# Performance work log

Measured on AMD Instinct MI355X. Metric: run time of the kernel, lower is better.

Reference implementation:

```python
import jax, jax.numpy as jnp
import numpy as np

REF_MIC_IDX = 0
LOAD = 0.001 / np.sqrt(2.0)  # diagonal loading added to BOTH real and imag parts in the torch code


def setup_inputs() -> dict:
    key = jax.random.key(0)
    k1, k2, k3 = jax.random.split(key, 3)
    shape = (8, 2, 8, 600, 257)  # N, RI, C, T, F
    return {
        "mixture": jax.random.normal(k1, shape, dtype=jnp.float32),
        "target": jax.random.normal(k2, shape, dtype=jnp.float32),
        "noise": jax.random.normal(k3, shape, dtype=jnp.float32),
    }


def _to_complex(x):
    # (N, 2, C, T, F) RI-stacked -> (N, C, T, F) complex
    return jax.lax.complex(x[:, 0], x[:, 1])


def reference(mixture, target, noise):
    N, _, C, T, F = mixture.shape
    y = _to_complex(mixture)  # (N, C, T, F)
    v = _to_complex(noise)
    cdtype = y.dtype

    # Time-averaged spatial covariance: sum_t V V^H / T -> (N, F, C, C)
    # (fused; the original materializes per-frame C x C matrices then sums)
    phi_v = jnp.einsum("nctf,ndtf->nfcd", v, jnp.conj(v)) / T
    phi_y = jnp.einsum("nctf,ndtf->nfcd", y, jnp.conj(y)) / T

    eye = jnp.eye(C, dtype=cdtype)
    # torch adds LOAD*eye to both real and imag slices -> complex (1+1j)*LOAD*eye
    phi_v = phi_v + (LOAD * (1.0 + 1.0j)) * eye

    G = jnp.linalg.inv(phi_v) @ phi_y  # (N, F, C, C)

    # l = trace(G) - C, where torch subtracts scalar C from both RI parts
    l = jnp.trace(G, axis1=-2, axis2=-1) - (C * (1.0 + 1.0j))  # (N, F)

    # H = (1/l) * (G - I) e_ref  -> column ref_mic_idx of (G - I)
    Ge = (G - eye)[..., :, REF_MIC_IDX]  # (N, F, C)
    H = Ge / l[..., None]  # (N, F, C)

    # Beamform: X(n,t,f) = sum_c conj(H)_{n,f,c} * y_{n,c,t,f}
    X = jnp.einsum("nfc,nctf->ntf", jnp.conj(H), y)  # (N, T, F)

    # Output in RI-stacked form with singleton channel: (N, 2, 1, T, F)
    est = jnp.stack([jnp.real(X), jnp.imag(X)], axis=1)[:, :, None]
    return est
```

## Files before the change

### kernel.cpp

```cpp
#include <hip/hip_runtime.h>


constexpr int N_  = 8;
constexpr int C_  = 8;
constexpr int T_  = 600;
constexpr int F_  = 257;
constexpr int TF_  = T_ * F_;
constexpr int CTF_ = C_ * TF_;
constexpr int NSTR_ = 2 * CTF_;
constexpr int NF_  = N_ * F_;
constexpr int NPAIR_ = 36;
constexpr float LOADC_ = 7.0710678118654755e-4f;
constexpr float INV_T_ = 1.0f / 600.0f;

struct cx { float r, i; };
__device__ __forceinline__ cx cmul(cx a, cx b) { return {a.r*b.r - a.i*b.i, a.r*b.i + a.i*b.r}; }
__device__ __forceinline__ cx csub(cx a, cx b) { return {a.r - b.r, a.i - b.i}; }
__device__ __forceinline__ cx cconj(cx a) { return {a.r, -a.i}; }
__device__ __forceinline__ cx cinv(cx a) {
    float id = 1.0f / (a.r*a.r + a.i*a.i);
    return {a.r*id, -a.i*id};
}
__device__ __forceinline__ cx cmadd(cx acc, cx a, cx b) {
    acc.r += a.r*b.r - a.i*b.i;
    acc.i += a.r*b.i + a.i*b.r;
    return acc;
}

template<int TSPLIT>
__global__ __launch_bounds__(64, 1) void cov_partial(
        const float* __restrict__ mix, const float* __restrict__ noi,
        float* __restrict__ part) {
    constexpr int TCHUNK = T_ / TSPLIT;
    constexpr int PIPE = 4;
    static_assert(TCHUNK > PIPE, "pipeline deeper than chunk");

    int f = blockIdx.x * 64 + threadIdx.x;
    if (f >= F_) return;
    int n = blockIdx.y;
    int z = blockIdx.z;
    int m = z & 1;
    int chunk = z >> 1;
    const float* src = m ? mix : noi;
    const float* pt = src + (size_t)n * NSTR_ + f + (size_t)(chunk * TCHUNK) * F_;

    float reB[PIPE][C_], imB[PIPE][C_];
#pragma unroll
    for (int s = 0; s < PIPE; ++s) {
        const float* pn = pt + (size_t)s * F_;
#pragma unroll
        for (int c = 0; c < C_; ++c) {
            reB[s][c] = pn[(size_t)c * TF_];
            imB[s][c] = pn[(size_t)c * TF_ + CTF_];
        }
    }

    float accr[NPAIR_], acci[NPAIR_];
#pragma unroll
    for (int p = 0; p < NPAIR_; ++p) { accr[p] = 0.f; acci[p] = 0.f; }

#pragma unroll
    for (int tt = 0; tt < TCHUNK; ++tt) {
        const int s = tt % PIPE;
        float re[C_], im[C_];
#pragma unroll
        for (int c = 0; c < C_; ++c) { re[c] = reB[s][c]; im[c] = imB[s][c]; }

        if (tt + PIPE < TCHUNK) {
            const float* pn = pt + (size_t)(tt + PIPE) * F_;
#pragma unroll
            for (int c = 0; c < C_; ++c) {
                reB[s][c] = pn[(size_t)c * TF_];
                imB[s][c] = pn[(size_t)c * TF_ + CTF_];
            }
        }

        int p = 0;
#pragma unroll
        for (int c = 0; c < C_; ++c) {
#pragma unroll
            for (int d = 0; d <= c; ++d, ++p) {
                accr[p] += re[c]*re[d] + im[c]*im[d];
                acci[p] += im[c]*re[d] - re[c]*im[d];
            }
        }
    }

    float* out = part + (size_t)((m * TSPLIT + chunk) * 72) * NF_ + n * F_ + f;
#pragma unroll
    for (int p = 0; p < NPAIR_; ++p) {
        out[(size_t)(2*p)   * NF_] = accr[p];
        out[(size_t)(2*p+1) * NF_] = acci[p];
    }
}

__global__ __launch_bounds__(256) void reduce_cov(float* __restrict__ part, int tsplit) {
    int flat = blockIdx.x * 256 + threadIdx.x;
    constexpr int NQ4 = NF_ / 4;
    if (flat >= 2 * 72 * NQ4) return;
    int idx4 = flat % NQ4;
    int z = flat / NQ4;
    int m = z / 72;
    int q = z % 72;
    const float4* p4 = (const float4*)(part) + ((size_t)((m * tsplit) * 72 + q) * NF_) / 4 + idx4;
    float4 s = {0.f, 0.f, 0.f, 0.f};
    for (int ch = 0; ch < tsplit; ++ch) {
        float4 v = p4[(size_t)(ch * 72) * NF_ / 4];
        s.x += v.x; s.y += v.y; s.z += v.z; s.w += v.w;
    }
    *(float4*)((float*)part + (size_t)((m * tsplit) * 72 + q) * NF_ + idx4 * 4) = s;
}

__global__ __launch_bounds__(64, 1) void solve_w(
        const float* __restrict__ part, float* __restrict__ W, size_t yBase) {
    int idx = blockIdx.x * 64 + threadIdx.x;
    if (idx >= NF_) return;

    const float* pv = part + idx;
    const float* py = part + yBase + idx;

    cx M[64];
#pragma unroll
    for (int c = 0; c < 8; ++c) {
#pragma unroll
        for (int d = 0; d <= c; ++d) {
            int p = c*(c+1)/2 + d;
            cx val = { pv[(size_t)(2*p) * NF_] * INV_T_,
                       pv[(size_t)(2*p+1) * NF_] * INV_T_ };
            if (d == c) { val.r += LOADC_; val.i += LOADC_; }
            M[c*8 + d] = val;
            if (d < c) M[d*8 + c] = cconj(val);
        }
    }

#pragma unroll
    for (int k = 0; k < 8; ++k) {
        cx p = cinv(M[k*8 + k]);
        M[k*8 + k] = p;
#pragma unroll
        for (int j = 0; j < 8; ++j) {
            if (j != k) M[k*8 + j] = cmul(M[k*8 + j], p);
        }
#pragma unroll
        for (int i = 0; i < 8; ++i) {
            if (i == k) continue;
            cx fkt = M[i*8 + k];
#pragma unroll
            for (int j = 0; j < 8; ++j) {
                if (j != k) M[i*8 + j] = csub(M[i*8 + j], cmul(fkt, M[k*8 + j]));
            }
            cx t = cmul(fkt, p);
            M[i*8 + k] = { -t.r, -t.i };
        }
    }

    cx tr = {0.f, 0.f};
    cx g0[8];
#pragma unroll
    for (int c = 0; c < 8; ++c) g0[c] = (cx){0.f, 0.f};

#pragma unroll
    for (int a = 0; a < 8; ++a) {
#pragma unroll
        for (int b = 0; b <= a; ++b) {
            int p = a*(a+1)/2 + b;
            cx yv = { py[(size_t)(2*p) * NF_] * INV_T_,
                      py[(size_t)(2*p+1) * NF_] * INV_T_ };
            tr = cmadd(tr, M[b*8 + a], yv);
            if (a != b) tr = cmadd(tr, M[a*8 + b], cconj(yv));
            if (b == 0) {
#pragma unroll
                for (int i = 0; i < 8; ++i) g0[i] = cmadd(g0[i], M[i*8 + a], yv);
            }
        }
    }

    cx l = { tr.r - 8.0f, tr.i - 8.0f };
    float iden = 1.0f / (l.r*l.r + l.i*l.i);

    float* w = W + (size_t)idx * 16;
#pragma unroll
    for (int c = 0; c < 8; ++c) {
        cx ge = g0[c];
        if (c == 0) ge.r -= 1.0f;
        w[2*c]     = (ge.r*l.r + ge.i*l.i) * iden;
        w[2*c + 1] = (ge.r*l.i - ge.i*l.r) * iden;
    }
}

__global__ __launch_bounds__(256) void beamform(
        const float* __restrict__ mix, const float* __restrict__ W,
        float* __restrict__ out) {
    int n = blockIdx.y;
    int j = blockIdx.x * 256 + threadIdx.x;
    if (j >= TF_) return;
    int f = j % F_;

    const float4* w4 = (const float4*)(W + (size_t)(n * F_ + f) * 16);
    float4 q0 = w4[0], q1 = w4[1], q2 = w4[2], q3 = w4[3];
    float wv[16] = { q0.x, q0.y, q0.z, q0.w,
                     q1.x, q1.y, q1.z, q1.w,
                     q2.x, q2.y, q2.z, q2.w,
                     q3.x, q3.y, q3.z, q3.w };

    const float* base = mix + (size_t)n * NSTR_ + j;
    float xr = 0.f, xi = 0.f;
#pragma unroll
    for (int c = 0; c < C_; ++c) {
        float yr = base[(size_t)c * TF_];
        float yi = base[(size_t)c * TF_ + CTF_];
        float wr = wv[2*c], wi = wv[2*c + 1];
        xr += wr*yr - wi*yi;
        xi += wr*yi + wi*yr;
    }
    float* op = out + (size_t)n * (2 * TF_);
    op[j]       = xr;
    op[TF_ + j] = xi;
}

extern "C" void kernel_launch(void* const* d_in, const int* in_sizes, int n_in,
                              void* d_out, int out_size, void* d_ws, size_t ws_size,
                              hipStream_t stream) {
    const float* mix = (const float*)d_in[0];
    const float* noi = (const float*)d_in[2];

    const size_t need25 = ((size_t)2 * 25 * 72 * NF_ + (size_t)16 * NF_) * 4;
    float* part = (float*)d_ws;
    int tsplit;
    if (ws_size >= need25) {
        tsplit = 25;
        cov_partial<25><<<dim3(5, N_, 2 * 25), 64, 0, stream>>>(mix, noi, part);
    } else {
        tsplit = 15;
        cov_partial<15><<<dim3(5, N_, 2 * 15), 64, 0, stream>>>(mix, noi, part);
    }
    float* W = part + (size_t)2 * tsplit * 72 * NF_;

    reduce_cov<<<dim3((2 * 72 * (NF_ / 4) + 255) / 256), 256, 0, stream>>>(part, tsplit);
    solve_w<<<dim3((NF_ + 63) / 64), 64, 0, stream>>>(part, W, (size_t)tsplit * 72 * NF_);
    beamform<<<dim3((TF_ + 255) / 256, N_), 256, 0, stream>>>(mix, W, (float*)d_out);
}
```

Measured before the change: 281.6 us.

## Stream covariance inputs through an async global-to-LDS ring buffer

The covariance kernel used to prefetch four time frames into registers. It now issues direct global-to-LDS loads into a three-stage shared-memory ring, with manual vmcnt and lgkmcnt waits between stages. The intent is to keep more loads in flight per wave while freeing registers held by the prefetch buffers, since this one-wave-per-block kernel is bound by memory latency. The fallback time split changes from 15 to 20 so the chunk length divides evenly by the ring depth. The trade-off is hand-written wait counts that must match the number of loads each stage issues, which is fragile, plus extra LDS read traffic.

```diff
diff --git a/kernel.cpp b/kernel.cpp
--- a/kernel.cpp
+++ b/kernel.cpp
@@ -1,4 +1,5 @@
 #include <hip/hip_runtime.h>
+#include <stdint.h>
 
 
 constexpr int N_  = 8;
@@ -27,54 +28,57 @@
     return acc;
 }
 
+__device__ __forceinline__ void gload_lds4(const float* g, float* l) {
+    __builtin_amdgcn_global_load_lds(
+        (const __attribute__((address_space(1))) void*)g,
+        (__attribute__((address_space(3))) void*)l,
+        4, 0, 0);
+}
+
+#define VMWAIT(N) asm volatile("s_waitcnt vmcnt(" #N ")" ::: "memory")
+#define LGKM0()   asm volatile("s_waitcnt lgkmcnt(0)" ::: "memory")
+
 template<int TSPLIT>
 __global__ __launch_bounds__(64, 1) void cov_partial(
         const float* __restrict__ mix, const float* __restrict__ noi,
         float* __restrict__ part) {
     constexpr int TCHUNK = T_ / TSPLIT;
-    constexpr int PIPE = 4;
-    static_assert(TCHUNK > PIPE, "pipeline deeper than chunk");
-
-    int f = blockIdx.x * 64 + threadIdx.x;
+    constexpr int P = 3;
+    static_assert(TCHUNK % P == 0 && TCHUNK > P, "ring/chunk mismatch");
+
+    __shared__ float S[P][16][64];
+
+    const int lane = threadIdx.x;
+    const int f = blockIdx.x * 64 + lane;
     if (f >= F_) return;
-    int n = blockIdx.y;
-    int z = blockIdx.z;
-    int m = z & 1;
-    int chunk = z >> 1;
-    const float* src = m ? mix : noi;
-    const float* pt = src + (size_t)n * NSTR_ + f + (size_t)(chunk * TCHUNK) * F_;
-
-    float reB[PIPE][C_], imB[PIPE][C_];
-#pragma unroll
-    for (int s = 0; s < PIPE; ++s) {
-        const float* pn = pt + (size_t)s * F_;
+    const int n = blockIdx.y;
+    const int z = blockIdx.z;
+    const int m = z & 1;
+    const int chunk = z >> 1;
+    const float* src = (m ? mix : noi) + (size_t)n * NSTR_
+                     + (size_t)(chunk * TCHUNK) * F_ + f;
+
+    auto stage = [&](int s, int t) {
+        const float* pg = src + (size_t)t * F_;
+        float* lp = &S[s][0][0];
 #pragma unroll
         for (int c = 0; c < C_; ++c) {
-            reB[s][c] = pn[(size_t)c * TF_];
-            imB[s][c] = pn[(size_t)c * TF_ + CTF_];
-        }
-    }
+            gload_lds4(pg + (size_t)c * TF_,        lp + (2*c)   * 64);
+            gload_lds4(pg + (size_t)c * TF_ + CTF_, lp + (2*c+1) * 64);
+        }
+    };
 
     float accr[NPAIR_], acci[NPAIR_];
 #pragma unroll
     for (int p = 0; p < NPAIR_; ++p) { accr[p] = 0.f; acci[p] = 0.f; }
 
-#pragma unroll
-    for (int tt = 0; tt < TCHUNK; ++tt) {
-        const int s = tt % PIPE;
+    auto consume = [&](int s) {
         float re[C_], im[C_];
 #pragma unroll
-        for (int c = 0; c < C_; ++c) { re[c] = reB[s][c]; im[c] = imB[s][c]; }
-
-        if (tt + PIPE < TCHUNK) {
-            const float* pn = pt + (size_t)(tt + PIPE) * F_;
-#pragma unroll
-            for (int c = 0; c < C_; ++c) {
-                reB[s][c] = pn[(size_t)c * TF_];
-                imB[s][c] = pn[(size_t)c * TF_ + CTF_];
-            }
-        }
-
+        for (int c = 0; c < C_; ++c) {
+            re[c] = S[s][2*c][lane];
+            im[c] = S[s][2*c+1][lane];
+        }
         int p = 0;
 #pragma unroll
         for (int c = 0; c < C_; ++c) {
@@ -84,7 +88,18 @@
                 acci[p] += im[c]*re[d] - re[c]*im[d];
             }
         }
-    }
+    };
+
+    stage(0, 0); stage(1, 1); stage(2, 2);
+
+    for (int tb = 0; tb < TCHUNK - P; tb += P) {
+        VMWAIT(32); consume(0); LGKM0(); stage(0, tb + 3);
+        VMWAIT(32); consume(1); LGKM0(); stage(1, tb + 4);
+        VMWAIT(32); consume(2); LGKM0(); stage(2, tb + 5);
+    }
+    VMWAIT(32); consume(0);
+    VMWAIT(16); consume(1);
+    VMWAIT(0);  consume(2);
 
     float* out = part + (size_t)((m * TSPLIT + chunk) * 72) * NF_ + n * F_ + f;
 #pragma unroll
@@ -231,8 +246,8 @@
         tsplit = 25;
         cov_partial<25><<<dim3(5, N_, 2 * 25), 64, 0, stream>>>(mix, noi, part);
     } else {
-        tsplit = 15;
-        cov_partial<15><<<dim3(5, N_, 2 * 15), 64, 0, stream>>>(mix, noi, part);
+        tsplit = 20;
+        cov_partial<20><<<dim3(5, N_, 2 * 20), 64, 0, stream>>>(mix, noi, part);
     }
     float* W = part + (size_t)2 * tsplit * 72 * NF_;
 
```

Result: no change. 282.3 us (+0.2%).
